# Kernel tuning notes

Measured on AMD Instinct MI355X. Metric: run time of the kernel, lower is better.

## Reference

```python
import jax, jax.numpy as jnp
import numpy as np

B, S, D, H = 2, 2048, 1024, 16
HD = D // H


def setup_inputs() -> dict:
    key = jax.random.key(0)
    ks = jax.random.split(key, 6)
    scale = D ** -0.5
    return {
        "x": jax.random.normal(ks[0], (B, S, D), dtype=jnp.float32),
        "attn_mask": jnp.ones((B, S), dtype=bool),
        "wq": jax.random.normal(ks[1], (D, D), dtype=jnp.float32) * scale,
        "wk": jax.random.normal(ks[2], (D, D), dtype=jnp.float32) * scale,
        "wv": jax.random.normal(ks[3], (D, D), dtype=jnp.float32) * scale,
        "wo": jax.random.normal(ks[4], (D, D), dtype=jnp.float32) * scale,
        "bo": jax.random.normal(ks[5], (D,), dtype=jnp.float32) * 0.01,
    }


def reference(x, attn_mask, wq, wk, wv, wo, bo):
    b, s, d = x.shape
    # torch Linear: y = x @ W.T
    q = (x @ wq.T).reshape(b, s, H, HD).transpose(0, 2, 1, 3)  # (b,h,s,hd)
    k = (x @ wk.T).reshape(b, s, H, HD).transpose(0, 2, 1, 3)
    v = (x @ wv.T).reshape(b, s, H, HD).transpose(0, 2, 1, 3)
    scores = jnp.einsum("bhqd,bhkd->bhqk", q, k) * (HD ** -0.5)
    causal = jnp.triu(jnp.ones((s, s), dtype=bool), k=1)  # True above diagonal
    mask = causal[None, None, :, :] | (~attn_mask)[:, None, None, :]
    mask_value = jnp.finfo(scores.dtype).min / 2
    scores = jnp.where(mask, mask_value, scores)
    att = jax.nn.softmax(scores, axis=-1)
    ctx = jnp.einsum("bhqk,bhkd->bhqd", att, v)
    ctx = ctx.transpose(0, 2, 1, 3).reshape(b, s, d)
    return ctx @ wo.T + bo
```

## Files before the change

### kernel.cpp

```cpp
#include <hip/hip_runtime.h>
#include <stdint.h>

#define SEQ   2048
#define DMODEL 1024
#define NHEAD 16
#define HDIM  64
#define MTOT  4096

typedef short s16x8 __attribute__((ext_vector_type(8)));
typedef float f32x4 __attribute__((ext_vector_type(4)));
typedef float f32x16 __attribute__((ext_vector_type(16)));
typedef unsigned u32x4 __attribute__((ext_vector_type(4)));

#define LOG2E 1.44269504088896340736f

#if __has_builtin(__builtin_amdgcn_exp2f)
#define EXP2(x) __builtin_amdgcn_exp2f(x)
#else
#define EXP2(x) exp2f(x)
#endif

__device__ __forceinline__ short f2bf(float f) {
  union { float f; unsigned u; } v; v.f = f;
  unsigned u = v.u + 0x7fff + ((v.u >> 16) & 1);
  return (short)(u >> 16);
}

__device__ __forceinline__ void async_cp16(const void* g, void* l) {
  __builtin_amdgcn_global_load_lds(
      (const __attribute__((address_space(1))) void*)g,
      (__attribute__((address_space(3))) void*)l, 16, 0, 0);
}

__device__ __forceinline__ f32x4 mfma16(s16x8 a, s16x8 b, f32x4 c) {
  return __builtin_amdgcn_mfma_f32_16x16x32_bf16(a, b, c, 0, 0, 0);
}
__device__ __forceinline__ f32x16 mfma32(s16x8 a, s16x8 b, f32x16 c) {
  return __builtin_amdgcn_mfma_f32_32x32x16_bf16(a, b, c, 0, 0, 0);
}

__global__ __launch_bounds__(256) void cast_kernel(
    const float* __restrict__ x,  const float* __restrict__ wq,
    const float* __restrict__ wk, const float* __restrict__ wv,
    const float* __restrict__ wo,
    short* __restrict__ xb,  short* __restrict__ wqb,
    short* __restrict__ wkb, short* __restrict__ wvb, short* __restrict__ wob) {
  int i = blockIdx.x * 256 + threadIdx.x;
  const float4* src; short* dst; int off;
  const int XN = 1 << 20, WN = 1 << 18;
  if (i < XN)            { src = (const float4*)x;  dst = xb;  off = i; }
  else if (i < XN + WN)  { src = (const float4*)wq; dst = wqb; off = i - XN; }
  else if (i < XN + 2*WN){ src = (const float4*)wk; dst = wkb; off = i - XN - WN; }
  else if (i < XN + 3*WN){ src = (const float4*)wv; dst = wvb; off = i - XN - 2*WN; }
  else                   { src = (const float4*)wo; dst = wob; off = i - XN - 3*WN; }
  float4 v = src[off];
  short4 o; o.x = f2bf(v.x); o.y = f2bf(v.y); o.z = f2bf(v.z); o.w = f2bf(v.w);
  *(short4*)(dst + off * 4) = o;
}

__global__ __launch_bounds__(512, 2) void qkv_gemm(
    const short* __restrict__ xb,  const short* __restrict__ wqb,
    const short* __restrict__ wkb, const short* __restrict__ wvb,
    short* __restrict__ Q, short* __restrict__ K, short* __restrict__ Vt) {
  __shared__ short SMEM[32768];
  short (*Abuf)[4096] = reinterpret_cast<short (*)[4096]>(SMEM);
  short (*Bbuf)[3][4096] = reinterpret_cast<short (*)[3][4096]>(SMEM + 8192);
  const int tid = threadIdx.x;
  const int w = tid >> 6, lane = tid & 63;
  const int c = lane & 15, g = lane >> 4;
  const int wm = w >> 2, wn = w & 3;
  const int n0 = blockIdx.x * 128, m0 = blockIdx.y * 128;
  const int srow = lane >> 2, schunk = lane & 3;

  f32x4 acc[3][4][2] = {};

#define QKV_STAGE(KT, BS)                                                      \
  {                                                                            \
    async_cp16(xb + (m0 + w * 16 + srow) * 1024 + (KT) * 32 + schunk * 8,      \
               &Abuf[BS][w * 512]);                                            \
    async_cp16(wqb + (n0 + w * 16 + srow) * 1024 + (KT) * 32 + schunk * 8,     \
               &Bbuf[BS][0][w * 512]);                                         \
    async_cp16(wkb + (n0 + w * 16 + srow) * 1024 + (KT) * 32 + schunk * 8,     \
               &Bbuf[BS][1][w * 512]);                                         \
    async_cp16(wvb + (n0 + w * 16 + srow) * 1024 + (KT) * 32 + schunk * 8,     \
               &Bbuf[BS][2][w * 512]);                                         \
  }

  QKV_STAGE(0, 0)
  for (int kt = 0; kt < 32; ++kt) {
    __syncthreads();
    if (kt + 1 < 32) { QKV_STAGE(kt + 1, (kt + 1) & 1) }
    const int cur = kt & 1;
    s16x8 a[4];
#pragma unroll
    for (int t = 0; t < 4; ++t)
      a[t] = *(const s16x8*)&Abuf[cur][(wm * 64 + t * 16 + c) * 32 + g * 8];
#pragma unroll
    for (int z = 0; z < 3; ++z) {
      s16x8 b[2];
#pragma unroll
      for (int u = 0; u < 2; ++u)
        b[u] = *(const s16x8*)&Bbuf[cur][z][(wn * 32 + u * 16 + c) * 32 + g * 8];
#pragma unroll
      for (int t = 0; t < 4; ++t)
#pragma unroll
        for (int u = 0; u < 2; ++u)
          acc[z][t][u] = mfma16(a[t], b[u], acc[z][t][u]);
    }
  }

  short* E = SMEM;
  const int b0 = m0 >> 11, sbase = m0 & 2047, hgb = n0 >> 6;

#pragma unroll
  for (int z = 0; z < 3; ++z) {
    __syncthreads();
    if (z == 2) {
#pragma unroll
      for (int t = 0; t < 4; ++t)
#pragma unroll
        for (int u = 0; u < 2; ++u) {
          int col = wn * 32 + u * 16 + c;
          int m = wm * 64 + t * 16 + g * 4;
          int phys = (m >> 3) ^ (col & 15);
          short4 o;
          o.x = f2bf(acc[z][t][u][0]); o.y = f2bf(acc[z][t][u][1]);
          o.z = f2bf(acc[z][t][u][2]); o.w = f2bf(acc[z][t][u][3]);
          *(short4*)&E[col * 128 + phys * 8 + (m & 7)] = o;
        }
      __syncthreads();
#pragma unroll
      for (int p = 0; p < 4; ++p) {
        int R = p * 32 + (tid >> 4);
        int j = tid & 15;
        int phys = j ^ (R & 15);
        s16x8 v = *(const s16x8*)&E[R * 128 + phys * 8];
        int hloc = R >> 6, hd = R & 63;
        *(s16x8*)&Vt[(((b0 * 16 + hgb + hloc) * 64 + hd) * 2048) + sbase + j * 8] = v;
      }
    } else {
      const float scale = (z == 0) ? 0.125f * LOG2E : 1.0f;
#pragma unroll
      for (int t = 0; t < 4; ++t)
#pragma unroll
        for (int u = 0; u < 2; ++u)
#pragma unroll
          for (int r = 0; r < 4; ++r) {
            int m = wm * 64 + t * 16 + g * 4 + r;
            int col = wn * 32 + u * 16 + c;
            int phys = (col >> 3) ^ ((m >> 2) & 15);
            E[m * 128 + phys * 8 + (col & 7)] = f2bf(acc[z][t][u][r] * scale);
          }
      __syncthreads();
      short* __restrict__ dst = (z == 0) ? Q : K;
#pragma unroll
      for (int p = 0; p < 4; ++p) {
        int R = p * 64 + (tid >> 3);
        int j = tid & 7;
        int m = R >> 1, hloc = R & 1;
        int phys = (hloc * 8 + j) ^ ((m >> 2) & 15);
        s16x8 v = *(const s16x8*)&E[m * 128 + phys * 8];
        *(s16x8*)&dst[(((b0 * 16 + hgb + hloc) * 2048) + sbase + m) * 64 + j * 8] = v;
      }
    }
  }
}

#define STAGE_K(KT, BS)                                                        \
  _Pragma("unroll") for (int j = 0; j < 4; ++j) {                              \
    int idx = w * 4 + j;                                                       \
    int ks = idx >> 3, p = idx & 7;                                            \
    async_cp16(Kg + ((KT) * 128 + p * 16 + srow) * 64 + ks * 32 + sw8,         \
               &Kbuf[BS][ks][p * 512]);                                        \
  }
#define STAGE_V(KT)                                                            \
  _Pragma("unroll") for (int j = 0; j < 4; ++j) {                              \
    int idx = w * 4 + j;                                                       \
    int ks2 = idx >> 2, p = idx & 3;                                           \
    async_cp16(Vg + (p * 16 + srow) * 2048 + (KT) * 128 + ks2 * 32 + sw8,      \
               &Vlds[ks2][p * 512]);                                           \
  }

__global__ __launch_bounds__(256, 3) void attn_kernel(
    const short* __restrict__ Q, const short* __restrict__ K,
    const short* __restrict__ Vt, short* __restrict__ ctx) {
  __shared__ short Kbuf[2][2][128 * 32];
  __shared__ short Vlds[4][64 * 32];
  __shared__ float Llds[4][32];

  const int tid = threadIdx.x;
  const int w = tid >> 6, lane = tid & 63;
  const int n31 = lane & 31, h = lane >> 5;
  int bx = blockIdx.x;
  if (blockIdx.y >= 16) bx = 15 - bx;
  const int bh = blockIdx.y;
  const int qbase = bx * 128 + w * 32;
  const short* __restrict__ Qg = Q + bh * (SEQ * HDIM);
  const short* __restrict__ Kg = K + bh * (SEQ * HDIM);
  const short* __restrict__ Vg = Vt + bh * (SEQ * HDIM);
  const int srow = lane >> 2, schunk = lane & 3;
  const int sw8 = (schunk ^ ((srow >> 1) & 3)) * 8;
  const int rsw = (n31 >> 1) & 3;

  s16x8 qf[4];
#pragma unroll
  for (int ch = 0; ch < 4; ++ch)
    qf[ch] = *(const s16x8*)&Qg[(qbase + n31) * 64 + ch * 16 + h * 8];

  float l_run = 0.f;
  f32x16 oacc[2] = {};

  STAGE_K(0, 0)
  for (int kt = 0; kt <= bx; ++kt) {
    __syncthreads();
    if (kt < bx) { STAGE_K(kt + 1, (kt + 1) & 1) }
    STAGE_V(kt)

    const bool diag = (kt == bx);
    const int mtmax = diag ? w : 3;
    const short (*Kc)[128 * 32] = Kbuf[kt & 1];

    unsigned pk[4][8];
#pragma unroll
    for (int mt = 0; mt < 4; ++mt) {
      if (mt > mtmax) break;
      f32x16 st = {};
#pragma unroll
      for (int ch = 0; ch < 4; ++ch) {
        s16x8 ka = *(const s16x8*)
            &Kc[ch >> 1][(mt * 32 + n31) * 32 + ((((ch & 1) * 2 + h) ^ rsw) * 8)];
        st = mfma32(ka, qf[ch], st);
      }
      if (diag && mt == w) {
#pragma unroll
        for (int reg = 0; reg < 16; ++reg) {
          int krow = (reg & 3) + 8 * (reg >> 2) + 4 * h;
          if (krow > n31) st[reg] = -1e30f;
        }
      }
#pragma unroll
      for (int i = 0; i < 8; ++i) {
        float p0 = EXP2(st[2 * i]);
        float p1 = EXP2(st[2 * i + 1]);
        unsigned t0 = __float_as_uint(p0) & 0xffff0000u;
        unsigned t1 = __float_as_uint(p1) & 0xffff0000u;
        l_run += __uint_as_float(t0);
        l_run += __uint_as_float(t1);
        pk[mt][i] = (t0 >> 16) | t1;
      }
    }

    __syncthreads();

#pragma unroll
    for (int mt = 0; mt < 4; ++mt) {
      if (mt > mtmax) break;
#pragma unroll
      for (int kb2 = 0; kb2 < 2; ++kb2) {
        const int kb = mt * 2 + kb2;
        const unsigned q0 = pk[mt][kb2 * 4 + 0], q1 = pk[mt][kb2 * 4 + 1];
        const unsigned q2 = pk[mt][kb2 * 4 + 2], q3 = pk[mt][kb2 * 4 + 3];
        const unsigned x0 = __shfl_xor(q0, 32), x1 = __shfl_xor(q1, 32);
        const unsigned x2 = __shfl_xor(q2, 32), x3 = __shfl_xor(q3, 32);
        u32x4 av;
        av.x = h ? x2 : q0;
        av.y = h ? x3 : q1;
        av.z = h ? q2 : x0;
        av.w = h ? q3 : x1;
        s16x8 pa = __builtin_bit_cast(s16x8, av);
#pragma unroll
        for (int u = 0; u < 2; ++u) {
          s16x8 vf = *(const s16x8*)
              &Vlds[kb >> 1][(u * 32 + n31) * 32 + ((((kb & 1) * 2 + h) ^ rsw) * 8)];
          oacc[u] = mfma32(pa, vf, oacc[u]);
        }
      }
    }
  }

  float lf = l_run + __shfl_xor(l_run, 32);
  if (h == 0) Llds[w][n31] = lf;
  float inv[4][4];
#pragma unroll
  for (int gi = 0; gi < 4; ++gi) {
    float4 lv = *(const float4*)&Llds[w][gi * 8 + 4 * h];
    inv[gi][0] = 1.0f / lv.x; inv[gi][1] = 1.0f / lv.y;
    inv[gi][2] = 1.0f / lv.z; inv[gi][3] = 1.0f / lv.w;
  }

  const int b = bh >> 4, hh = bh & 15;
#pragma unroll
  for (int u = 0; u < 2; ++u)
#pragma unroll
    for (int gi = 0; gi < 4; ++gi)
#pragma unroll
      for (int ri = 0; ri < 4; ++ri) {
        int q = qbase + 8 * gi + 4 * h + ri;
        int hd = u * 32 + n31;
        ctx[(b * 2048 + q) * 1024 + hh * 64 + hd] =
            f2bf(oacc[u][gi * 4 + ri] * inv[gi][ri]);
      }
}

__global__ __launch_bounds__(256) void out_gemm(
    const short* __restrict__ ctx, const short* __restrict__ wob,
    const float* __restrict__ bo, float* __restrict__ out) {
  __shared__ short Abuf[2][128 * 32];
  __shared__ short Bbuf[2][64 * 32];
  const int tid = threadIdx.x;
  const int w = tid >> 6, lane = tid & 63;
  const int c = lane & 15, g = lane >> 4;
  const int wm = w >> 1, wn = w & 1;
  const int n0 = blockIdx.x * 64, m0 = blockIdx.y * 128;
  const int srow = lane >> 2, schunk = lane & 3;

  f32x4 acc[4][2] = {};

#define OUT_STAGE(KT, BS)                                                      \
  {                                                                            \
    _Pragma("unroll") for (int j = 0; j < 2; ++j) {                            \
      int p = w * 2 + j;                                                       \
      async_cp16(ctx + (m0 + p * 16 + srow) * 1024 + (KT) * 32 + schunk * 8,   \
                 &Abuf[BS][p * 512]);                                          \
    }                                                                          \
    async_cp16(wob + (n0 + w * 16 + srow) * 1024 + (KT) * 32 + schunk * 8,     \
               &Bbuf[BS][w * 512]);                                            \
  }

  OUT_STAGE(0, 0)
  for (int kt = 0; kt < 32; ++kt) {
    __syncthreads();
    if (kt + 1 < 32) { OUT_STAGE(kt + 1, (kt + 1) & 1) }
    const int cur = kt & 1;
    s16x8 a[4], b[2];
#pragma unroll
    for (int t = 0; t < 4; ++t)
      a[t] = *(const s16x8*)&Abuf[cur][(wm * 64 + t * 16 + c) * 32 + g * 8];
#pragma unroll
    for (int u = 0; u < 2; ++u)
      b[u] = *(const s16x8*)&Bbuf[cur][(wn * 32 + u * 16 + c) * 32 + g * 8];
#pragma unroll
    for (int t = 0; t < 4; ++t)
#pragma unroll
      for (int u = 0; u < 2; ++u)
        acc[t][u] = mfma16(a[t], b[u], acc[t][u]);
  }

#pragma unroll
  for (int t = 0; t < 4; ++t)
#pragma unroll
    for (int u = 0; u < 2; ++u) {
      int col = n0 + wn * 32 + u * 16 + c;
      float bias = bo[col];
#pragma unroll
      for (int r = 0; r < 4; ++r) {
        int m = m0 + wm * 64 + t * 16 + g * 4 + r;
        out[m * 1024 + col] = acc[t][u][r] + bias;
      }
    }
}

extern "C" void kernel_launch(void* const* d_in, const int* in_sizes, int n_in,
                              void* d_out, int out_size, void* d_ws, size_t ws_size,
                              hipStream_t stream) {
  const float* x  = (const float*)d_in[0];
  const float* wq = (const float*)d_in[2];
  const float* wk = (const float*)d_in[3];
  const float* wv = (const float*)d_in[4];
  const float* wo = (const float*)d_in[5];
  const float* bo = (const float*)d_in[6];

  char* ws = (char*)d_ws;
  short* xb  = (short*)(ws);
  short* wqb = (short*)(ws + (size_t)( 8 << 20));
  short* wkb = (short*)(ws + (size_t)(10 << 20));
  short* wvb = (short*)(ws + (size_t)(12 << 20));
  short* wob = (short*)(ws + (size_t)(14 << 20));
  short* Qb  = (short*)(ws + (size_t)(16 << 20));
  short* Kb  = (short*)(ws + (size_t)(24 << 20));
  short* Vtb = (short*)(ws + (size_t)(32 << 20));
  short* ctx = (short*)(ws + (size_t)(40 << 20));
  float* out = (float*)d_out;

  cast_kernel<<<dim3(8192), dim3(256), 0, stream>>>(x, wq, wk, wv, wo,
                                                    xb, wqb, wkb, wvb, wob);
  qkv_gemm<<<dim3(8, 32), dim3(512), 0, stream>>>(xb, wqb, wkb, wvb,
                                                  Qb, Kb, Vtb);
  attn_kernel<<<dim3(16, 32), dim3(256), 0, stream>>>(Qb, Kb, Vtb, ctx);
  out_gemm<<<dim3(16, 32), dim3(256), 0, stream>>>(ctx, wob, bo, out);
}
```

Before: 183.1 us.

## Double-buffer V tiles, use permlane32 swap, add setprio, remap grids

The attention kernel now double-buffers V in LDS so the next K and V tiles are prefetched together. This removes the mid-iteration barrier. Cross-half shuffles are replaced with v_permlane32_swap, and bf16 packing uses a single perm instruction. MFMA blocks in all GEMMs are wrapped in s_setprio raises, and the grid indexing of the attention and output GEMMs is swapped, with a new causal-balance pairing across the y dimension. The larger LDS footprint lowers the occupancy hint from 3 to 2 blocks.

```diff
diff --git a/kernel.cpp b/kernel.cpp
--- a/kernel.cpp
+++ b/kernel.cpp
@@ -37,6 +37,15 @@
 }
 __device__ __forceinline__ f32x16 mfma32(s16x8 a, s16x8 b, f32x16 c) {
   return __builtin_amdgcn_mfma_f32_32x32x16_bf16(a, b, c, 0, 0, 0);
+}
+
+__device__ __forceinline__ void plane32swap(unsigned& a, unsigned& b) {
+#if __has_builtin(__builtin_amdgcn_permlane32_swap)
+  auto r = __builtin_amdgcn_permlane32_swap(a, b, false, false);
+  a = r[0]; b = r[1];
+#else
+  asm("v_permlane32_swap_b32 %0, %1" : "+v"(a), "+v"(b));
+#endif
 }
 
 __global__ __launch_bounds__(256) void cast_kernel(
@@ -101,11 +110,13 @@
 #pragma unroll
       for (int u = 0; u < 2; ++u)
         b[u] = *(const s16x8*)&Bbuf[cur][z][(wn * 32 + u * 16 + c) * 32 + g * 8];
+      __builtin_amdgcn_s_setprio(1);
 #pragma unroll
       for (int t = 0; t < 4; ++t)
 #pragma unroll
         for (int u = 0; u < 2; ++u)
           acc[z][t][u] = mfma16(a[t], b[u], acc[z][t][u]);
+      __builtin_amdgcn_s_setprio(0);
     }
   }
 
@@ -173,27 +184,27 @@
     async_cp16(Kg + ((KT) * 128 + p * 16 + srow) * 64 + ks * 32 + sw8,         \
                &Kbuf[BS][ks][p * 512]);                                        \
   }
-#define STAGE_V(KT)                                                            \
+#define STAGE_V(KT, BS)                                                        \
   _Pragma("unroll") for (int j = 0; j < 4; ++j) {                              \
     int idx = w * 4 + j;                                                       \
     int ks2 = idx >> 2, p = idx & 3;                                           \
     async_cp16(Vg + (p * 16 + srow) * 2048 + (KT) * 128 + ks2 * 32 + sw8,      \
-               &Vlds[ks2][p * 512]);                                           \
-  }
-
-__global__ __launch_bounds__(256, 3) void attn_kernel(
+               &Vlds[BS][ks2][p * 512]);                                       \
+  }
+
+__global__ __launch_bounds__(256, 2) void attn_kernel(
     const short* __restrict__ Q, const short* __restrict__ K,
     const short* __restrict__ Vt, short* __restrict__ ctx) {
   __shared__ short Kbuf[2][2][128 * 32];
-  __shared__ short Vlds[4][64 * 32];
+  __shared__ short Vlds[2][4][64 * 32];
   __shared__ float Llds[4][32];
 
   const int tid = threadIdx.x;
   const int w = tid >> 6, lane = tid & 63;
   const int n31 = lane & 31, h = lane >> 5;
-  int bx = blockIdx.x;
-  if (blockIdx.y >= 16) bx = 15 - bx;
-  const int bh = blockIdx.y;
+  const int bh = blockIdx.x;
+  int bx = blockIdx.y;
+  if (bx >= 8) bx = 23 - bx;
   const int qbase = bx * 128 + w * 32;
   const short* __restrict__ Qg = Q + bh * (SEQ * HDIM);
   const short* __restrict__ Kg = K + bh * (SEQ * HDIM);
@@ -211,26 +222,29 @@
   f32x16 oacc[2] = {};
 
   STAGE_K(0, 0)
+  STAGE_V(0, 0)
   for (int kt = 0; kt <= bx; ++kt) {
     __syncthreads();
-    if (kt < bx) { STAGE_K(kt + 1, (kt + 1) & 1) }
-    STAGE_V(kt)
+    if (kt < bx) { STAGE_K(kt + 1, (kt + 1) & 1) STAGE_V(kt + 1, (kt + 1) & 1) }
 
     const bool diag = (kt == bx);
     const int mtmax = diag ? w : 3;
     const short (*Kc)[128 * 32] = Kbuf[kt & 1];
+    const short (*Vc)[64 * 32] = Vlds[kt & 1];
 
     unsigned pk[4][8];
 #pragma unroll
     for (int mt = 0; mt < 4; ++mt) {
       if (mt > mtmax) break;
       f32x16 st = {};
+      __builtin_amdgcn_s_setprio(1);
 #pragma unroll
       for (int ch = 0; ch < 4; ++ch) {
         s16x8 ka = *(const s16x8*)
             &Kc[ch >> 1][(mt * 32 + n31) * 32 + ((((ch & 1) * 2 + h) ^ rsw) * 8)];
         st = mfma32(ka, qf[ch], st);
       }
+      __builtin_amdgcn_s_setprio(0);
       if (diag && mt == w) {
 #pragma unroll
         for (int reg = 0; reg < 16; ++reg) {
@@ -242,15 +256,13 @@
       for (int i = 0; i < 8; ++i) {
         float p0 = EXP2(st[2 * i]);
         float p1 = EXP2(st[2 * i + 1]);
-        unsigned t0 = __float_as_uint(p0) & 0xffff0000u;
-        unsigned t1 = __float_as_uint(p1) & 0xffff0000u;
-        l_run += __uint_as_float(t0);
-        l_run += __uint_as_float(t1);
-        pk[mt][i] = (t0 >> 16) | t1;
+        unsigned u0 = __float_as_uint(p0);
+        unsigned u1 = __float_as_uint(p1);
+        l_run += __uint_as_float(u0 & 0xffff0000u);
+        l_run += __uint_as_float(u1 & 0xffff0000u);
+        pk[mt][i] = __builtin_amdgcn_perm(u1, u0, 0x07060302u);
       }
     }
-
-    __syncthreads();
 
 #pragma unroll
     for (int mt = 0; mt < 4; ++mt) {
@@ -258,22 +270,20 @@
 #pragma unroll
       for (int kb2 = 0; kb2 < 2; ++kb2) {
         const int kb = mt * 2 + kb2;
-        const unsigned q0 = pk[mt][kb2 * 4 + 0], q1 = pk[mt][kb2 * 4 + 1];
-        const unsigned q2 = pk[mt][kb2 * 4 + 2], q3 = pk[mt][kb2 * 4 + 3];
-        const unsigned x0 = __shfl_xor(q0, 32), x1 = __shfl_xor(q1, 32);
-        const unsigned x2 = __shfl_xor(q2, 32), x3 = __shfl_xor(q3, 32);
-        u32x4 av;
-        av.x = h ? x2 : q0;
-        av.y = h ? x3 : q1;
-        av.z = h ? q2 : x0;
-        av.w = h ? q3 : x1;
+        unsigned q0 = pk[mt][kb2 * 4 + 0], q1 = pk[mt][kb2 * 4 + 1];
+        unsigned q2 = pk[mt][kb2 * 4 + 2], q3 = pk[mt][kb2 * 4 + 3];
+        plane32swap(q0, q2);
+        plane32swap(q1, q3);
+        u32x4 av; av.x = q0; av.y = q1; av.z = q2; av.w = q3;
         s16x8 pa = __builtin_bit_cast(s16x8, av);
+        __builtin_amdgcn_s_setprio(1);
 #pragma unroll
         for (int u = 0; u < 2; ++u) {
           s16x8 vf = *(const s16x8*)
-              &Vlds[kb >> 1][(u * 32 + n31) * 32 + ((((kb & 1) * 2 + h) ^ rsw) * 8)];
+              &Vc[kb >> 1][(u * 32 + n31) * 32 + ((((kb & 1) * 2 + h) ^ rsw) * 8)];
           oacc[u] = mfma32(pa, vf, oacc[u]);
         }
+        __builtin_amdgcn_s_setprio(0);
       }
     }
   }
@@ -311,7 +321,7 @@
   const int w = tid >> 6, lane = tid & 63;
   const int c = lane & 15, g = lane >> 4;
   const int wm = w >> 1, wn = w & 1;
-  const int n0 = blockIdx.x * 64, m0 = blockIdx.y * 128;
+  const int n0 = blockIdx.y * 64, m0 = blockIdx.x * 128;
   const int srow = lane >> 2, schunk = lane & 3;
 
   f32x4 acc[4][2] = {};
@@ -339,11 +349,13 @@
 #pragma unroll
     for (int u = 0; u < 2; ++u)
       b[u] = *(const s16x8*)&Bbuf[cur][(wn * 32 + u * 16 + c) * 32 + g * 8];
+    __builtin_amdgcn_s_setprio(1);
 #pragma unroll
     for (int t = 0; t < 4; ++t)
 #pragma unroll
       for (int u = 0; u < 2; ++u)
         acc[t][u] = mfma16(a[t], b[u], acc[t][u]);
+    __builtin_amdgcn_s_setprio(0);
   }
 
 #pragma unroll
@@ -386,6 +398,6 @@
                                                     xb, wqb, wkb, wvb, wob);
   qkv_gemm<<<dim3(8, 32), dim3(512), 0, stream>>>(xb, wqb, wkb, wvb,
                                                   Qb, Kb, Vtb);
-  attn_kernel<<<dim3(16, 32), dim3(256), 0, stream>>>(Qb, Kb, Vtb, ctx);
-  out_gemm<<<dim3(16, 32), dim3(256), 0, stream>>>(ctx, wob, bo, out);
-}
+  attn_kernel<<<dim3(32, 16), dim3(256), 0, stream>>>(Qb, Kb, Vtb, ctx);
+  out_gemm<<<dim3(32, 16), dim3(256), 0, stream>>>(ctx, wob, bo, out);
+}
```

Result: no change. 180.1 us (-1.6%).
